# Optimization experiments

Hardware: AMD Instinct MI355X
Metric: run time of the kernel (lower is better)

The kernel has to match this reference:

```python
import jax, jax.numpy as jnp
import numpy as np

CUTOFF = 10.0
NUM_GAUSSIANS = 50
LOG2 = float(np.log(2.0))
PI = float(np.pi)


def ssp(v):
    # shifted softplus: softplus(x) - log(2)
    return jax.nn.softplus(v) - LOG2


def setup_inputs() -> dict:
    key = jax.random.key(0)
    ks = jax.random.split(key, 16)
    N, E, H, F, G, L = 10000, 320000, 128, 128, NUM_GAUSSIANS, 6
    s = 0.08  # param scale to keep activations stable over 6 layers
    return {
        "x": jax.random.randint(ks[0], (N,), 0, 100),
        "edge_index": jax.random.randint(ks[1], (2, E), 0, N),
        "edge_dist": jax.random.uniform(ks[2], (E,), jnp.float32) * CUTOFF,
        "emb": jax.random.normal(ks[3], (100, H), jnp.float32) * s,
        "mlp_w1": jax.random.normal(ks[4], (L, G, F), jnp.float32) * s,
        "mlp_b1": jnp.zeros((L, F), jnp.float32),
        "mlp_w2": jax.random.normal(ks[5], (L, F, F), jnp.float32) * s,
        "mlp_b2": jnp.zeros((L, F), jnp.float32),
        "lin1_w": jax.random.normal(ks[6], (L, H, F), jnp.float32) * s,
        "lin2_w": jax.random.normal(ks[7], (L, F, H), jnp.float32) * s,
        "lin2_b": jnp.zeros((L, H), jnp.float32),
        "lin_w": jax.random.normal(ks[8], (L, H, H), jnp.float32) * s,
        "lin_b": jnp.zeros((L, H), jnp.float32),
        "out1_w": jax.random.normal(ks[9], (H, H // 2), jnp.float32) * s,
        "out1_b": jnp.zeros((H // 2,), jnp.float32),
        "out2_w": jax.random.normal(ks[10], (H // 2, H // 2), jnp.float32) * s,
        "out2_b": jnp.zeros((H // 2,), jnp.float32),
        "ro_w": jax.random.normal(ks[11], (H // 2, 12), jnp.float32) * s,
        "ro_b": jnp.zeros((12,), jnp.float32),
    }


def reference(x, edge_index, edge_dist, emb, mlp_w1, mlp_b1, mlp_w2, mlp_b2,
              lin1_w, lin2_w, lin2_b, lin_w, lin_b,
              out1_w, out1_b, out2_w, out2_b, ro_w, ro_b):
    N = x.shape[0]
    L = mlp_w1.shape[0]
    src, dst = edge_index[0], edge_index[1]

    h = emb[x]  # [N, H]

    # Gaussian smearing of distances -> [E, G]
    offset = jnp.linspace(0.0, CUTOFF, NUM_GAUSSIANS)
    coeff = -0.5 / (offset[1] - offset[0]) ** 2
    ea = jnp.exp(coeff * (edge_dist[:, None] - offset[None, :]) ** 2)

    # cosine cutoff envelope C [E]
    C = 0.5 * (jnp.cos(edge_dist * PI / CUTOFF) + 1.0)

    for l in range(L):
        # per-edge filter: MLP(gaussian) * cutoff  -> [E, F]
        W = (ssp(ea @ mlp_w1[l] + mlp_b1[l]) @ mlp_w2[l] + mlp_b2[l]) * C[:, None]
        xf = h @ lin1_w[l]                      # [N, F] (lin1, no bias)
        msg = xf[src] * W                       # gather + elementwise [E, F]
        agg = jax.ops.segment_sum(msg, dst, num_segments=N)  # scatter-add
        conv = agg @ lin2_w[l] + lin2_b[l]      # [N, H]
        h = h + (ssp(conv) @ lin_w[l] + lin_b[l])

    t = ssp(h @ out1_w + out1_b)
    t = t @ out2_w + out2_b
    h_agg = jnp.sum(t, axis=0)                  # [H//2]
    return h_agg @ ro_w + ro_b                  # [12]
```

## Files before the change

kernel.cpp:

```cpp
#include <hip/hip_runtime.h>
#include <math.h>

#define E_NUM 320000
#define N_NUM 10000
#define NB8   (N_NUM / 8)
#define NB16  (N_NUM / 16)
#define TAB   2048

typedef unsigned short ushort_t;
typedef short short8_t __attribute__((ext_vector_type(8)));
typedef float f32x4    __attribute__((ext_vector_type(4)));

#define WP_O1   294912
#define WP_O2   303104
#define WP_W1T  307200
#define WP_W2T  356352
#define WP_TOT  454656

#define HB  1250
#define PB  ((WP_TOT + 255) / 256)
#define SCB 1250

__device__ __forceinline__ float ssp_f(float x) {
    return fmaxf(x, 0.f) + __logf(1.f + __expf(-fabsf(x))) - 0.69314718056f;
}

__device__ __forceinline__ float bf2f(ushort_t u) {
    union { unsigned int i; float f; } v;
    v.i = ((unsigned int)u) << 16;
    return v.f;
}
__device__ __forceinline__ ushort_t f2bf(float f) {
    union { float f; unsigned int i; } v;
    v.f = f;
    unsigned int u = v.i;
    unsigned int r = (u + 0x7FFFu + ((u >> 16) & 1u)) >> 16;
    return (ushort_t)r;
}

__global__ __launch_bounds__(256) void hist_pack_kernel(const int* __restrict__ ei,
                                                        int* __restrict__ counts,
                                                        const float* __restrict__ lin2_w,
                                                        const float* __restrict__ lin_w,
                                                        const float* __restrict__ lin1_w,
                                                        const float* __restrict__ o1w,
                                                        const float* __restrict__ o2w,
                                                        const float* __restrict__ mlp_w1,
                                                        const float* __restrict__ mlp_w2,
                                                        short* __restrict__ wpack) {
    if (blockIdx.x < HB) {
        int e = blockIdx.x * 256 + threadIdx.x;
        if (e < E_NUM) atomicAdd(&counts[ei[E_NUM + e]], 1);
        return;
    }
    int idx = (blockIdx.x - HB) * 256 + threadIdx.x;
    const int M128 = 16384;
    if (idx < 18 * M128) {
        int g = idx / M128, r = idx % M128;
        const float* src;
        if (g < 6) src = lin2_w + g * M128;
        else if (g < 12) src = lin_w + (g - 6) * M128;
        else src = lin1_w + (g - 12) * M128;
        int j = r & 7, L = (r >> 3) & 63, ks = (r >> 9) & 3, t = r >> 11;
        int n = t * 16 + (L & 15);
        int k = ks * 32 + (L >> 4) * 8 + j;
        wpack[idx] = (short)f2bf(src[k * 128 + n]);
    } else if (idx < WP_O2) {
        int r = idx - WP_O1;
        int j = r & 7, L = (r >> 3) & 63, ks = (r >> 9) & 3, t = r >> 11;
        int n = t * 16 + (L & 15);
        int k = ks * 32 + (L >> 4) * 8 + j;
        wpack[idx] = (short)f2bf(o1w[k * 64 + n]);
    } else if (idx < WP_W1T) {
        int r = idx - WP_O2;
        int j = r & 7, L = (r >> 3) & 63, ks = (r >> 9) & 1, t = r >> 10;
        int n = t * 16 + (L & 15);
        int k = ks * 32 + (L >> 4) * 8 + j;
        wpack[idx] = (short)f2bf(o2w[k * 64 + n]);
    } else if (idx < WP_W2T) {
        int r2 = idx - WP_W1T;
        int g = r2 / 8192, r = r2 % 8192;
        int j = r & 7, L = (r >> 3) & 63, ks = (r >> 9) & 1, t = r >> 10;
        int n = t * 16 + (L & 15);
        int k = ks * 32 + (L >> 4) * 8 + j;
        float v = (k < 50) ? mlp_w1[g * 6400 + k * 128 + n] : 0.f;
        wpack[idx] = (short)f2bf(v);
    } else if (idx < WP_TOT) {
        int r2 = idx - WP_W2T;
        int g = r2 / M128, r = r2 % M128;
        int j = r & 7, L = (r >> 3) & 63, ks = (r >> 9) & 3, t = r >> 11;
        int n = t * 16 + (L & 15);
        int k = ks * 32 + (L >> 4) * 8 + j;
        wpack[idx] = (short)f2bf(mlp_w2[g * M128 + k * 128 + n]);
    }
}

__global__ __launch_bounds__(1024) void scan_kernel(const int* __restrict__ counts,
                                                    int* __restrict__ offs,
                                                    int* __restrict__ cursor) {
    __shared__ int part[1024];
    const int tid = threadIdx.x;
    const int CH = 10;
    int base = tid * CH;
    int s = 0;
    #pragma unroll
    for (int i = 0; i < CH; ++i) {
        int idx = base + i;
        if (idx < N_NUM) s += counts[idx];
    }
    part[tid] = s;
    __syncthreads();
    for (int off = 1; off < 1024; off <<= 1) {
        int v = (tid >= off) ? part[tid - off] : 0;
        __syncthreads();
        part[tid] += v;
        __syncthreads();
    }
    int run = (tid > 0) ? part[tid - 1] : 0;
    #pragma unroll
    for (int i = 0; i < CH; ++i) {
        int idx = base + i;
        if (idx < N_NUM) {
            offs[idx] = run;
            cursor[idx] = run;
            run += counts[idx];
        }
    }
    if (tid == 1023) offs[N_NUM] = part[1023];
}

__global__ __launch_bounds__(256) void scatter_embed_kernel(const int* __restrict__ ei,
                                                            const float* __restrict__ dist,
                                                            int* __restrict__ cursor,
                                                            int* __restrict__ meta,
                                                            const int* __restrict__ x,
                                                            const float* __restrict__ emb,
                                                            const float* __restrict__ B,
                                                            float* __restrict__ h,
                                                            ushort_t* __restrict__ xf) {
    if (blockIdx.x < SCB) {
        int e = blockIdx.x * 256 + threadIdx.x;
        if (e >= E_NUM) return;
        int d = ei[E_NUM + e];
        int pos = atomicAdd(&cursor[d], 1);
        float t = dist[e] * ((float)(TAB - 1) / 10.0f);
        int i0 = (int)(t + 0.5f);
        if (i0 > TAB - 1) i0 = TAB - 1;
        meta[pos] = (i0 << 14) | ei[e];
        return;
    }
    __shared__ float AT[128][9];
    __shared__ int s_x[8];
    const int tid = threadIdx.x;
    const int n0 = (blockIdx.x - SCB) * 8;

    if (tid < 8) s_x[tid] = x[n0 + tid];
    __syncthreads();
    for (int i = tid; i < 8 * 128; i += 256) {
        int r = i >> 7, c = i & 127;
        float v = emb[s_x[r] * 128 + c];
        AT[c][r] = v;
        h[(size_t)(n0 + r) * 128 + c] = v;
    }
    __syncthreads();

    const int r  = tid & 7;
    const int c0 = (tid >> 3) * 4;
    float acc[4] = {0.f, 0.f, 0.f, 0.f};
    for (int k = 0; k < 128; k += 4) {
        float a[4];
        #pragma unroll
        for (int u = 0; u < 4; ++u) a[u] = AT[k + u][r];
        #pragma unroll
        for (int u = 0; u < 4; ++u) {
            float4 b = *(const float4*)(B + (size_t)(k + u) * 128 + c0);
            acc[0] = fmaf(a[u], b.x, acc[0]);
            acc[1] = fmaf(a[u], b.y, acc[1]);
            acc[2] = fmaf(a[u], b.z, acc[2]);
            acc[3] = fmaf(a[u], b.w, acc[3]);
        }
    }
    ushort4 o;
    o.x = f2bf(acc[0]); o.y = f2bf(acc[1]); o.z = f2bf(acc[2]); o.w = f2bf(acc[3]);
    *(ushort4*)(xf + (size_t)(n0 + r) * 128 + c0) = o;
}

__global__ __launch_bounds__(512) void table_kernel(const short* __restrict__ w1t,
                                                    const float* __restrict__ mlp_b1,
                                                    const short* __restrict__ w2t,
                                                    const float* __restrict__ mlp_b2,
                                                    ushort_t* __restrict__ tabB) {
    __shared__ short EA[16 * 72];
    __shared__ short HD[16 * 136];
    const int tid = threadIdx.x;
    const int wv = tid >> 6;
    const int lane = tid & 63;
    const int l = blockIdx.x >> 7;
    const int r0 = (blockIdx.x & 127) * 16;
    const float DG = 10.0f / (float)(TAB - 1);
    const float STEP = 10.0f / 49.0f;
    const float COEFF = -0.5f / (STEP * STEP);

    for (int i = tid; i < 16 * 64; i += 512) {
        int r = i >> 6, k = i & 63;
        float v = 0.f;
        if (k < 50) {
            float d = (float)(r0 + r) * DG;
            float t = d - (float)k * STEP;
            v = __expf(COEFF * t * t);
        }
        EA[r * 72 + k] = (short)f2bf(v);
    }
    __syncthreads();

    const int m = lane & 15, q = lane >> 4;

    {
        f32x4 acc = {0.f, 0.f, 0.f, 0.f};
        #pragma unroll
        for (int ks = 0; ks < 2; ++ks) {
            short8_t a = *(const short8_t*)(EA + m * 72 + ks * 32 + q * 8);
            short8_t b = *(const short8_t*)(w1t + l * 8192 + (wv * 2 + ks) * 512 + lane * 8);
            acc = __builtin_amdgcn_mfma_f32_16x16x32_bf16(a, b, acc, 0, 0, 0);
        }
        float bv = mlp_b1[l * 128 + wv * 16 + m];
        #pragma unroll
        for (int i = 0; i < 4; ++i)
            HD[(q * 4 + i) * 136 + wv * 16 + m] = (short)f2bf(ssp_f(acc[i] + bv));
    }
    __syncthreads();

    {
        f32x4 acc = {0.f, 0.f, 0.f, 0.f};
        #pragma unroll
        for (int ks = 0; ks < 4; ++ks) {
            short8_t a = *(const short8_t*)(HD + m * 136 + ks * 32 + q * 8);
            short8_t b = *(const short8_t*)(w2t + l * 16384 + (wv * 4 + ks) * 512 + lane * 8);
            acc = __builtin_amdgcn_mfma_f32_16x16x32_bf16(a, b, acc, 0, 0, 0);
        }
        int col = wv * 16 + m;
        float bv = mlp_b2[l * 128 + col];
        ushort_t* tl = tabB + (size_t)l * TAB * 128;
        #pragma unroll
        for (int i = 0; i < 4; ++i) {
            int row = r0 + q * 4 + i;
            float d = (float)row * DG;
            float C = 0.5f * (__cosf(d * 0.31415926535f) + 1.0f);
            tl[(size_t)row * 128 + col] = f2bf((acc[i] + bv) * C);
        }
    }
}

__device__ __forceinline__ void nacc8(short8_t x, short8_t t, float* o) {
    #pragma unroll
    for (int j = 0; j < 8; ++j)
        o[j] = fmaf(bf2f((ushort_t)x[j]), bf2f((ushort_t)t[j]), o[j]);
}

template <bool LAST>
__global__ __launch_bounds__(512) void layer_kernel(const int* __restrict__ offs,
                                                    const int* __restrict__ meta,
                                                    const ushort_t* __restrict__ xf,
                                                    const ushort_t* __restrict__ tabB,
                                                    const short* __restrict__ w2p,
                                                    const float* __restrict__ lin2_b,
                                                    const short* __restrict__ wlp,
                                                    const float* __restrict__ lin_b,
                                                    const short* __restrict__ w1p,
                                                    float* __restrict__ h,
                                                    ushort_t* __restrict__ xf_out,
                                                    const short* __restrict__ o1p,
                                                    const float* __restrict__ o1b,
                                                    const short* __restrict__ o2p,
                                                    const float* __restrict__ o2b,
                                                    float* __restrict__ gs) {
    __shared__ short A1[16 * 136];
    __shared__ short A2[16 * 136];
    __shared__ float P[16 * 128];
    __shared__ float red[4][64];
    const int tid = threadIdx.x;
    const int n0 = blockIdx.x * 16;
    const int wv = tid >> 6;
    const int lane = tid & 63;
    const int strm = wv >> 2;

    {
        const int qt = lane >> 4;
        const int c8 = (lane & 15) * 8;
        const int row = (wv & 3) * 4 + qt;
        const int node = n0 + row;
        int s0 = offs[node];
        int s1 = offs[node + 1];
        int mid = s0 + ((s1 - s0) >> 1);
        int e   = strm ? mid : s0;
        int end = strm ? s1  : mid;

        float accA[8] = {0.f, 0.f, 0.f, 0.f, 0.f, 0.f, 0.f, 0.f};
        float accB[8] = {0.f, 0.f, 0.f, 0.f, 0.f, 0.f, 0.f, 0.f};

        for (; e + 8 <= end; e += 8) {
            int m[8];
            #pragma unroll
            for (int u = 0; u < 8; ++u) m[u] = meta[e + u];
            short8_t xv[8], tv[8];
            #pragma unroll
            for (int u = 0; u < 8; ++u) {
                xv[u] = *(const short8_t*)(xf + (size_t)(m[u] & 0x3FFF) * 128 + c8);
                tv[u] = *(const short8_t*)(tabB + (size_t)((unsigned)m[u] >> 14) * 128 + c8);
            }
            #pragma unroll
            for (int u = 0; u < 8; ++u)
                nacc8(xv[u], tv[u], (u & 1) ? accB : accA);
        }
        for (; e + 4 <= end; e += 4) {
            int m[4];
            #pragma unroll
            for (int u = 0; u < 4; ++u) m[u] = meta[e + u];
            short8_t xv[4], tv[4];
            #pragma unroll
            for (int u = 0; u < 4; ++u) {
                xv[u] = *(const short8_t*)(xf + (size_t)(m[u] & 0x3FFF) * 128 + c8);
                tv[u] = *(const short8_t*)(tabB + (size_t)((unsigned)m[u] >> 14) * 128 + c8);
            }
            #pragma unroll
            for (int u = 0; u < 4; ++u)
                nacc8(xv[u], tv[u], (u & 1) ? accB : accA);
        }
        for (; e < end; ++e) {
            int mm = meta[e];
            short8_t xv = *(const short8_t*)(xf + (size_t)(mm & 0x3FFF) * 128 + c8);
            short8_t tv = *(const short8_t*)(tabB + (size_t)((unsigned)mm >> 14) * 128 + c8);
            nacc8(xv, tv, accA);
        }

        if (!strm) {
            #pragma unroll
            for (int j = 0; j < 8; ++j)
                P[row * 128 + c8 + j] = accA[j] + accB[j];
        }
        __syncthreads();
        if (strm) {
            short8_t out;
            #pragma unroll
            for (int j = 0; j < 8; ++j)
                out[j] = (short)f2bf(accA[j] + accB[j] + P[row * 128 + c8 + j]);
            *(short8_t*)&A1[row * 136 + c8] = out;
        }
    }
    __syncthreads();

    const int m = lane & 15, q = lane >> 4;
    const int t = wv;

    {
        f32x4 acc = {0.f, 0.f, 0.f, 0.f};
        #pragma unroll
        for (int ks = 0; ks < 4; ++ks) {
            short8_t a = *(const short8_t*)(A1 + m * 136 + ks * 32 + q * 8);
            short8_t b = *(const short8_t*)(w2p + (t * 4 + ks) * 512 + lane * 8);
            acc = __builtin_amdgcn_mfma_f32_16x16x32_bf16(a, b, acc, 0, 0, 0);
        }
        float bv = lin2_b[t * 16 + m];
        #pragma unroll
        for (int i = 0; i < 4; ++i)
            A2[(q * 4 + i) * 136 + t * 16 + m] = (short)f2bf(ssp_f(acc[i] + bv));
    }
    __syncthreads();

    {
        f32x4 acc = {0.f, 0.f, 0.f, 0.f};
        #pragma unroll
        for (int ks = 0; ks < 4; ++ks) {
            short8_t a = *(const short8_t*)(A2 + m * 136 + ks * 32 + q * 8);
            short8_t b = *(const short8_t*)(wlp + (t * 4 + ks) * 512 + lane * 8);
            acc = __builtin_amdgcn_mfma_f32_16x16x32_bf16(a, b, acc, 0, 0, 0);
        }
        float bv = lin_b[t * 16 + m];
        #pragma unroll
        for (int i = 0; i < 4; ++i) {
            int r = q * 4 + i;
            int grow = n0 + r;
            float h0 = h[(size_t)grow * 128 + t * 16 + m];
            float hn = h0 + acc[i] + bv;
            if (!LAST) h[(size_t)grow * 128 + t * 16 + m] = hn;
            A1[r * 136 + t * 16 + m] = (short)f2bf(hn);
        }
    }
    __syncthreads();

    if constexpr (!LAST) {
        f32x4 acc = {0.f, 0.f, 0.f, 0.f};
        #pragma unroll
        for (int ks = 0; ks < 4; ++ks) {
            short8_t a = *(const short8_t*)(A1 + m * 136 + ks * 32 + q * 8);
            short8_t b = *(const short8_t*)(w1p + (t * 4 + ks) * 512 + lane * 8);
            acc = __builtin_amdgcn_mfma_f32_16x16x32_bf16(a, b, acc, 0, 0, 0);
        }
        #pragma unroll
        for (int i = 0; i < 4; ++i) {
            int r = q * 4 + i;
            int grow = n0 + r;
            xf_out[(size_t)grow * 128 + t * 16 + m] = f2bf(acc[i]);
        }
    } else {
        if (wv < 4) {
            f32x4 acc = {0.f, 0.f, 0.f, 0.f};
            #pragma unroll
            for (int ks = 0; ks < 4; ++ks) {
                short8_t a = *(const short8_t*)(A1 + m * 136 + ks * 32 + q * 8);
                short8_t b = *(const short8_t*)(o1p + (wv * 4 + ks) * 512 + lane * 8);
                acc = __builtin_amdgcn_mfma_f32_16x16x32_bf16(a, b, acc, 0, 0, 0);
            }
            float bv = o1b[wv * 16 + m];
            #pragma unroll
            for (int i = 0; i < 4; ++i) {
                int r = q * 4 + i;
                A2[r * 136 + wv * 16 + m] = (short)f2bf(ssp_f(acc[i] + bv));
            }
        }
        __syncthreads();
        if (wv < 4) {
            f32x4 acc = {0.f, 0.f, 0.f, 0.f};
            #pragma unroll
            for (int ks = 0; ks < 2; ++ks) {
                short8_t a = *(const short8_t*)(A2 + m * 136 + ks * 32 + q * 8);
                short8_t b = *(const short8_t*)(o2p + (wv * 2 + ks) * 512 + lane * 8);
                acc = __builtin_amdgcn_mfma_f32_16x16x32_bf16(a, b, acc, 0, 0, 0);
            }
            float bv = o2b[wv * 16 + m];
            float part = acc[0] + acc[1] + acc[2] + acc[3] + 4.0f * bv;
            red[q][wv * 16 + m] = part;
        }
        __syncthreads();
        if (tid < 64) {
            float s = red[0][tid] + red[1][tid] + red[2][tid] + red[3][tid];
            atomicAdd(&gs[tid], s);
        }
    }
}

__global__ void final_kernel(const float* __restrict__ gs,
                             const float* __restrict__ ro_w,
                             const float* __restrict__ ro_b,
                             float* __restrict__ out) {
    int i = threadIdx.x;
    if (i < 12) {
        float s = ro_b[i];
        for (int k = 0; k < 64; ++k) s = fmaf(gs[k], ro_w[k * 12 + i], s);
        out[i] = s;
    }
}

extern "C" void kernel_launch(void* const* d_in, const int* in_sizes, int n_in,
                              void* d_out, int out_size, void* d_ws, size_t ws_size,
                              hipStream_t stream) {
    const int*   x      = (const int*)d_in[0];
    const int*   ei     = (const int*)d_in[1];
    const float* dist   = (const float*)d_in[2];
    const float* emb    = (const float*)d_in[3];
    const float* mlp_w1 = (const float*)d_in[4];
    const float* mlp_b1 = (const float*)d_in[5];
    const float* mlp_w2 = (const float*)d_in[6];
    const float* mlp_b2 = (const float*)d_in[7];
    const float* lin1_w = (const float*)d_in[8];
    const float* lin2_w = (const float*)d_in[9];
    const float* lin2_b = (const float*)d_in[10];
    const float* lin_w  = (const float*)d_in[11];
    const float* lin_b  = (const float*)d_in[12];
    const float* out1_w = (const float*)d_in[13];
    const float* out1_b = (const float*)d_in[14];
    const float* out2_w = (const float*)d_in[15];
    const float* out2_b = (const float*)d_in[16];
    const float* ro_w   = (const float*)d_in[17];
    const float* ro_b   = (const float*)d_in[18];
    float* out = (float*)d_out;

    char* base = (char*)d_ws;
    float*    h     = (float*)base;     base += (size_t)N_NUM * 128 * 4;
    ushort_t* tabB  = (ushort_t*)base;  base += (size_t)6 * TAB * 128 * 2;
    ushort_t* xf0   = (ushort_t*)base;  base += (size_t)N_NUM * 128 * 2;
    ushort_t* xf1   = (ushort_t*)base;  base += (size_t)N_NUM * 128 * 2;
    int*      meta  = (int*)base;       base += (size_t)E_NUM * 4;
    short*    wpack = (short*)base;     base += (size_t)WP_TOT * 2;
    float*    gs    = (float*)base;     base += 64 * 4;
    int*      offs  = (int*)base;       base += (N_NUM + 1) * 4;
    int*      cursor= (int*)base;       base += N_NUM * 4;
    int*      counts= (int*)base;       base += N_NUM * 4;

    hipMemsetAsync(counts, 0, N_NUM * sizeof(int), stream);
    hipMemsetAsync(gs, 0, 64 * sizeof(float), stream);

    hist_pack_kernel<<<HB + PB, 256, 0, stream>>>(
        ei, counts, lin2_w, lin_w, lin1_w, out1_w, out2_w, mlp_w1, mlp_w2, wpack);

    scan_kernel<<<1, 1024, 0, stream>>>(counts, offs, cursor);

    scatter_embed_kernel<<<SCB + NB8, 256, 0, stream>>>(
        ei, dist, cursor, meta, x, emb, lin1_w, h, xf0);

    table_kernel<<<6 * (TAB / 16), 512, 0, stream>>>(
        wpack + WP_W1T, mlp_b1, wpack + WP_W2T, mlp_b2, tabB);

    const short* o1p = wpack + WP_O1;
    const short* o2p = wpack + WP_O2;

    for (int l = 0; l < 6; ++l) {
        ushort_t* xin  = (l & 1) ? xf1 : xf0;
        ushort_t* xout = (l & 1) ? xf0 : xf1;
        const ushort_t* tl = tabB + (size_t)l * TAB * 128;
        const short* w2p = wpack + l * 16384;
        const short* wlp = wpack + (6 + l) * 16384;
        if (l < 5) {
            const short* w1p = wpack + (12 + l + 1) * 16384;
            layer_kernel<false><<<NB16, 512, 0, stream>>>(
                offs, meta, xin, tl,
                w2p, lin2_b + l * 128, wlp, lin_b + l * 128, w1p,
                h, xout, nullptr, nullptr, nullptr, nullptr, nullptr);
        } else {
            layer_kernel<true><<<NB16, 512, 0, stream>>>(
                offs, meta, xin, tl,
                w2p, lin2_b + l * 128, wlp, lin_b + l * 128, nullptr,
                h, nullptr, o1p, out1_b, o2p, out2_b, gs);
        }
    }

    final_kernel<<<1, 64, 0, stream>>>(gs, ro_w, ro_b, out);
}
```

Before: 325.5 us.

## Fuse scatter, filter table and embed kernels; prefetch edge metadata in aggregation

Merges the edge scatter, filter-table build and embedding/lin1 projection into one front kernel with block-range dispatch, removing a launch. The embedding projection moves from scalar FP32 FMAs to bf16 MFMA using the pre-packed lin1 weights. The layer aggregation loop now software-pipelines the next eight metadata loads ahead of the gathers, which raises register use. Some bounds checks are dropped because the sizes divide evenly.

```diff
diff --git a/kernel.cpp b/kernel.cpp
--- a/kernel.cpp
+++ b/kernel.cpp
@@ -3,7 +3,6 @@
 
 #define E_NUM 320000
 #define N_NUM 10000
-#define NB8   (N_NUM / 8)
 #define NB16  (N_NUM / 16)
 #define TAB   2048
 
@@ -19,7 +18,10 @@
 
 #define HB  1250
 #define PB  ((WP_TOT + 255) / 256)
-#define SCB 1250
+
+#define FK_SC 625
+#define FK_TB 768
+#define FK_EM NB16
 
 __device__ __forceinline__ float ssp_f(float x) {
     return fmaxf(x, 0.f) + __logf(1.f + __expf(-fabsf(x))) - 0.69314718056f;
@@ -50,7 +52,7 @@
                                                         short* __restrict__ wpack) {
     if (blockIdx.x < HB) {
         int e = blockIdx.x * 256 + threadIdx.x;
-        if (e < E_NUM) atomicAdd(&counts[ei[E_NUM + e]], 1);
+        atomicAdd(&counts[ei[E_NUM + e]], 1);
         return;
     }
     int idx = (blockIdx.x - HB) * 256 + threadIdx.x;
@@ -77,7 +79,7 @@
         int n = t * 16 + (L & 15);
         int k = ks * 32 + (L >> 4) * 8 + j;
         wpack[idx] = (short)f2bf(o2w[k * 64 + n]);
-    } else if (idx < WP_W2T) {
+    } else if (idx < WP_W1T + 6 * 8192 && idx >= WP_W1T) {
         int r2 = idx - WP_W1T;
         int g = r2 / 8192, r = r2 % 8192;
         int j = r & 7, L = (r >> 3) & 63, ks = (r >> 9) & 1, t = r >> 10;
@@ -129,18 +131,27 @@
     if (tid == 1023) offs[N_NUM] = part[1023];
 }
 
-__global__ __launch_bounds__(256) void scatter_embed_kernel(const int* __restrict__ ei,
-                                                            const float* __restrict__ dist,
-                                                            int* __restrict__ cursor,
-                                                            int* __restrict__ meta,
-                                                            const int* __restrict__ x,
-                                                            const float* __restrict__ emb,
-                                                            const float* __restrict__ B,
-                                                            float* __restrict__ h,
-                                                            ushort_t* __restrict__ xf) {
-    if (blockIdx.x < SCB) {
-        int e = blockIdx.x * 256 + threadIdx.x;
-        if (e >= E_NUM) return;
+__global__ __launch_bounds__(512) void front_kernel(const int* __restrict__ ei,
+                                                    const float* __restrict__ dist,
+                                                    int* __restrict__ cursor,
+                                                    int* __restrict__ meta,
+                                                    const short* __restrict__ w1t,
+                                                    const float* __restrict__ mlp_b1,
+                                                    const short* __restrict__ w2t,
+                                                    const float* __restrict__ mlp_b2,
+                                                    ushort_t* __restrict__ tabB,
+                                                    const int* __restrict__ x,
+                                                    const float* __restrict__ emb,
+                                                    const short* __restrict__ w1p0,
+                                                    float* __restrict__ h,
+                                                    ushort_t* __restrict__ xf) {
+    __shared__ short EA[16 * 72];
+    __shared__ short HD[16 * 136];
+    __shared__ int s_x[16];
+    const int tid = threadIdx.x;
+
+    if (blockIdx.x < FK_SC) {
+        int e = blockIdx.x * 512 + tid;
         int d = ei[E_NUM + e];
         int pos = atomicAdd(&cursor[d], 1);
         float t = dist[e] * ((float)(TAB - 1) / 10.0f);
@@ -149,104 +160,94 @@
         meta[pos] = (i0 << 14) | ei[e];
         return;
     }
-    __shared__ float AT[128][9];
-    __shared__ int s_x[8];
-    const int tid = threadIdx.x;
-    const int n0 = (blockIdx.x - SCB) * 8;
-
-    if (tid < 8) s_x[tid] = x[n0 + tid];
-    __syncthreads();
-    for (int i = tid; i < 8 * 128; i += 256) {
-        int r = i >> 7, c = i & 127;
-        float v = emb[s_x[r] * 128 + c];
-        AT[c][r] = v;
-        h[(size_t)(n0 + r) * 128 + c] = v;
-    }
-    __syncthreads();
-
-    const int r  = tid & 7;
-    const int c0 = (tid >> 3) * 4;
-    float acc[4] = {0.f, 0.f, 0.f, 0.f};
-    for (int k = 0; k < 128; k += 4) {
-        float a[4];
-        #pragma unroll
-        for (int u = 0; u < 4; ++u) a[u] = AT[k + u][r];
-        #pragma unroll
-        for (int u = 0; u < 4; ++u) {
-            float4 b = *(const float4*)(B + (size_t)(k + u) * 128 + c0);
-            acc[0] = fmaf(a[u], b.x, acc[0]);
-            acc[1] = fmaf(a[u], b.y, acc[1]);
-            acc[2] = fmaf(a[u], b.z, acc[2]);
-            acc[3] = fmaf(a[u], b.w, acc[3]);
-        }
-    }
-    ushort4 o;
-    o.x = f2bf(acc[0]); o.y = f2bf(acc[1]); o.z = f2bf(acc[2]); o.w = f2bf(acc[3]);
-    *(ushort4*)(xf + (size_t)(n0 + r) * 128 + c0) = o;
-}
-
-__global__ __launch_bounds__(512) void table_kernel(const short* __restrict__ w1t,
-                                                    const float* __restrict__ mlp_b1,
-                                                    const short* __restrict__ w2t,
-                                                    const float* __restrict__ mlp_b2,
-                                                    ushort_t* __restrict__ tabB) {
-    __shared__ short EA[16 * 72];
-    __shared__ short HD[16 * 136];
-    const int tid = threadIdx.x;
+
     const int wv = tid >> 6;
     const int lane = tid & 63;
-    const int l = blockIdx.x >> 7;
-    const int r0 = (blockIdx.x & 127) * 16;
-    const float DG = 10.0f / (float)(TAB - 1);
-    const float STEP = 10.0f / 49.0f;
-    const float COEFF = -0.5f / (STEP * STEP);
-
-    for (int i = tid; i < 16 * 64; i += 512) {
-        int r = i >> 6, k = i & 63;
-        float v = 0.f;
-        if (k < 50) {
-            float d = (float)(r0 + r) * DG;
-            float t = d - (float)k * STEP;
-            v = __expf(COEFF * t * t);
-        }
-        EA[r * 72 + k] = (short)f2bf(v);
-    }
-    __syncthreads();
-
     const int m = lane & 15, q = lane >> 4;
 
+    if (blockIdx.x < FK_SC + FK_TB) {
+        const int bt = blockIdx.x - FK_SC;
+        const int l = bt >> 7;
+        const int r0 = (bt & 127) * 16;
+        const float DG = 10.0f / (float)(TAB - 1);
+        const float STEP = 10.0f / 49.0f;
+        const float COEFF = -0.5f / (STEP * STEP);
+
+        for (int i = tid; i < 16 * 64; i += 512) {
+            int r = i >> 6, k = i & 63;
+            float v = 0.f;
+            if (k < 50) {
+                float d = (float)(r0 + r) * DG;
+                float t = d - (float)k * STEP;
+                v = __expf(COEFF * t * t);
+            }
+            EA[r * 72 + k] = (short)f2bf(v);
+        }
+        __syncthreads();
+
+        {
+            f32x4 acc = {0.f, 0.f, 0.f, 0.f};
+            #pragma unroll
+            for (int ks = 0; ks < 2; ++ks) {
+                short8_t a = *(const short8_t*)(EA + m * 72 + ks * 32 + q * 8);
+                short8_t b = *(const short8_t*)(w1t + l * 8192 + (wv * 2 + ks) * 512 + lane * 8);
+                acc = __builtin_amdgcn_mfma_f32_16x16x32_bf16(a, b, acc, 0, 0, 0);
+            }
+            float bv = mlp_b1[l * 128 + wv * 16 + m];
+            #pragma unroll
+            for (int i = 0; i < 4; ++i)
+                HD[(q * 4 + i) * 136 + wv * 16 + m] = (short)f2bf(ssp_f(acc[i] + bv));
+        }
+        __syncthreads();
+
+        {
+            f32x4 acc = {0.f, 0.f, 0.f, 0.f};
+            #pragma unroll
+            for (int ks = 0; ks < 4; ++ks) {
+                short8_t a = *(const short8_t*)(HD + m * 136 + ks * 32 + q * 8);
+                short8_t b = *(const short8_t*)(w2t + l * 16384 + (wv * 4 + ks) * 512 + lane * 8);
+                acc = __builtin_amdgcn_mfma_f32_16x16x32_bf16(a, b, acc, 0, 0, 0);
+            }
+            int col = wv * 16 + m;
+            float bv = mlp_b2[l * 128 + col];
+            ushort_t* tl = tabB + (size_t)l * TAB * 128;
+            #pragma unroll
+            for (int i = 0; i < 4; ++i) {
+                int row = r0 + q * 4 + i;
+                float d = (float)row * DG;
+                float C = 0.5f * (__cosf(d * 0.31415926535f) + 1.0f);
+                tl[(size_t)row * 128 + col] = f2bf((acc[i] + bv) * C);
+            }
+        }
+        return;
+    }
+
     {
-        f32x4 acc = {0.f, 0.f, 0.f, 0.f};
-        #pragma unroll
-        for (int ks = 0; ks < 2; ++ks) {
-            short8_t a = *(const short8_t*)(EA + m * 72 + ks * 32 + q * 8);
-            short8_t b = *(const short8_t*)(w1t + l * 8192 + (wv * 2 + ks) * 512 + lane * 8);
-            acc = __builtin_amdgcn_mfma_f32_16x16x32_bf16(a, b, acc, 0, 0, 0);
-        }
-        float bv = mlp_b1[l * 128 + wv * 16 + m];
-        #pragma unroll
-        for (int i = 0; i < 4; ++i)
-            HD[(q * 4 + i) * 136 + wv * 16 + m] = (short)f2bf(ssp_f(acc[i] + bv));
-    }
-    __syncthreads();
-
-    {
+        const int n0 = (blockIdx.x - FK_SC - FK_TB) * 16;
+        if (tid < 16) s_x[tid] = x[n0 + tid];
+        __syncthreads();
+        {
+            int r = tid >> 5;
+            int c4 = (tid & 31) * 4;
+            float4 v = *(const float4*)(emb + (size_t)s_x[r] * 128 + c4);
+            *(float4*)(h + (size_t)(n0 + r) * 128 + c4) = v;
+            short4 o;
+            o.x = (short)f2bf(v.x); o.y = (short)f2bf(v.y);
+            o.z = (short)f2bf(v.z); o.w = (short)f2bf(v.w);
+            *(short4*)(HD + r * 136 + c4) = o;
+        }
+        __syncthreads();
         f32x4 acc = {0.f, 0.f, 0.f, 0.f};
         #pragma unroll
         for (int ks = 0; ks < 4; ++ks) {
             short8_t a = *(const short8_t*)(HD + m * 136 + ks * 32 + q * 8);
-            short8_t b = *(const short8_t*)(w2t + l * 16384 + (wv * 4 + ks) * 512 + lane * 8);
+            short8_t b = *(const short8_t*)(w1p0 + (wv * 4 + ks) * 512 + lane * 8);
             acc = __builtin_amdgcn_mfma_f32_16x16x32_bf16(a, b, acc, 0, 0, 0);
         }
-        int col = wv * 16 + m;
-        float bv = mlp_b2[l * 128 + col];
-        ushort_t* tl = tabB + (size_t)l * TAB * 128;
         #pragma unroll
         for (int i = 0; i < 4; ++i) {
-            int row = r0 + q * 4 + i;
-            float d = (float)row * DG;
-            float C = 0.5f * (__cosf(d * 0.31415926535f) + 1.0f);
-            tl[(size_t)row * 128 + col] = f2bf((acc[i] + bv) * C);
+            int grow = n0 + q * 4 + i;
+            xf[(size_t)grow * 128 + wv * 16 + m] = f2bf(acc[i]);
         }
     }
 }
@@ -298,33 +299,47 @@
         float accA[8] = {0.f, 0.f, 0.f, 0.f, 0.f, 0.f, 0.f, 0.f};
         float accB[8] = {0.f, 0.f, 0.f, 0.f, 0.f, 0.f, 0.f, 0.f};
 
-        for (; e + 8 <= end; e += 8) {
-            int m[8];
-            #pragma unroll
-            for (int u = 0; u < 8; ++u) m[u] = meta[e + u];
+        int mc[8];
+        bool have = (e + 8 <= end);
+        if (have) {
+            #pragma unroll
+            for (int u = 0; u < 8; ++u) mc[u] = meta[e + u];
+        }
+        while (have) {
+            bool nxt = (e + 16 <= end);
+            int mn[8];
+            if (nxt) {
+                #pragma unroll
+                for (int u = 0; u < 8; ++u) mn[u] = meta[e + 8 + u];
+            }
             short8_t xv[8], tv[8];
             #pragma unroll
             for (int u = 0; u < 8; ++u) {
-                xv[u] = *(const short8_t*)(xf + (size_t)(m[u] & 0x3FFF) * 128 + c8);
-                tv[u] = *(const short8_t*)(tabB + (size_t)((unsigned)m[u] >> 14) * 128 + c8);
+                xv[u] = *(const short8_t*)(xf + (size_t)(mc[u] & 0x3FFF) * 128 + c8);
+                tv[u] = *(const short8_t*)(tabB + (size_t)((unsigned)mc[u] >> 14) * 128 + c8);
             }
             #pragma unroll
             for (int u = 0; u < 8; ++u)
                 nacc8(xv[u], tv[u], (u & 1) ? accB : accA);
-        }
-        for (; e + 4 <= end; e += 4) {
-            int m[4];
-            #pragma unroll
-            for (int u = 0; u < 4; ++u) m[u] = meta[e + u];
+            #pragma unroll
+            for (int u = 0; u < 8; ++u) mc[u] = mn[u];
+            e += 8;
+            have = nxt;
+        }
+        if (e + 4 <= end) {
+            int mm[4];
+            #pragma unroll
+            for (int u = 0; u < 4; ++u) mm[u] = meta[e + u];
             short8_t xv[4], tv[4];
             #pragma unroll
             for (int u = 0; u < 4; ++u) {
-                xv[u] = *(const short8_t*)(xf + (size_t)(m[u] & 0x3FFF) * 128 + c8);
-                tv[u] = *(const short8_t*)(tabB + (size_t)((unsigned)m[u] >> 14) * 128 + c8);
+                xv[u] = *(const short8_t*)(xf + (size_t)(mm[u] & 0x3FFF) * 128 + c8);
+                tv[u] = *(const short8_t*)(tabB + (size_t)((unsigned)mm[u] >> 14) * 128 + c8);
             }
             #pragma unroll
             for (int u = 0; u < 4; ++u)
                 nacc8(xv[u], tv[u], (u & 1) ? accB : accA);
+            e += 4;
         }
         for (; e < end; ++e) {
             int mm = meta[e];
@@ -495,11 +510,10 @@
 
     scan_kernel<<<1, 1024, 0, stream>>>(counts, offs, cursor);
 
-    scatter_embed_kernel<<<SCB + NB8, 256, 0, stream>>>(
-        ei, dist, cursor, meta, x, emb, lin1_w, h, xf0);
-
-    table_kernel<<<6 * (TAB / 16), 512, 0, stream>>>(
-        wpack + WP_W1T, mlp_b1, wpack + WP_W2T, mlp_b2, tabB);
+    front_kernel<<<FK_SC + FK_TB + FK_EM, 512, 0, stream>>>(
+        ei, dist, cursor, meta,
+        wpack + WP_W1T, mlp_b1, wpack + WP_W2T, mlp_b2, tabB,
+        x, emb, wpack + 12 * 16384, h, xf0);
 
     const short* o1p = wpack + WP_O1;
     const short* o2p = wpack + WP_O2;
```

Result: faster. 288.3 us (-11.4%).
